# Kernel optimization log

Measured on AMD Instinct MI355X. Metric: run time of the kernel, lower is better.

Reference implementation:

```python
import jax, jax.numpy as jnp
import numpy as np

N_EDGES = 2_000_000
IN, HID, OUT = 10, 128, 4

# 4-bit narrow signed weight range: [-7, 7]; 4-bit unsigned act range: [0, 15]
W_QMAX = 7.0
A_QMAX = 15.0


def quant_weight(W):
    # NarrowIntQuant + MaxStatsScaling: per-tensor scale = max|W| / 7
    s = jnp.max(jnp.abs(W)) / W_QMAX
    return jnp.clip(jnp.round(W / s), -W_QMAX, W_QMAX) * s


def quant_act_relu(x, s):
    # QuantReLU with UintQuant: relu then uint4 fake-quant with per-tensor scale s
    x = jax.nn.relu(x)
    return jnp.clip(jnp.round(x / s), 0.0, A_QMAX) * s


def setup_inputs() -> dict:
    key = jax.random.key(0)
    ks = jax.random.split(key, 9)
    m = jax.random.normal(ks[0], (N_EDGES, IN), dtype=jnp.float32)
    W1 = jax.random.normal(ks[1], (HID, IN), dtype=jnp.float32) * (1.0 / np.sqrt(IN))
    b1 = jax.random.normal(ks[2], (HID,), dtype=jnp.float32) * 0.01
    W2 = jax.random.normal(ks[3], (HID, HID), dtype=jnp.float32) * (1.0 / np.sqrt(HID))
    b2 = jax.random.normal(ks[4], (HID,), dtype=jnp.float32) * 0.01
    W3 = jax.random.normal(ks[5], (OUT, HID), dtype=jnp.float32) * (1.0 / np.sqrt(HID))
    b3 = jax.random.normal(ks[6], (OUT,), dtype=jnp.float32) * 0.01
    # runtime-percentile act scales ~ typical pre-act magnitude / 15
    s_act1 = jax.random.uniform(ks[7], (1,), dtype=jnp.float32, minval=0.05, maxval=0.3)
    s_act2 = jax.random.uniform(ks[8], (1,), dtype=jnp.float32, minval=0.05, maxval=0.3)
    return {"m": m, "W1": W1, "b1": b1, "W2": W2, "b2": b2,
            "W3": W3, "b3": b3, "s_act1": s_act1, "s_act2": s_act2}


def reference(m, W1, b1, W2, b2, W3, b3, s_act1, s_act2):
    h = m @ quant_weight(W1).T + b1                 # [N, HID]
    h = quant_act_relu(h, s_act1[0])
    h = h @ quant_weight(W2).T + b2                 # [N, HID]
    h = quant_act_relu(h, s_act2[0])
    out = h @ quant_weight(W3).T + b3               # [N, OUT]
    return out
```

## Files before the change

### kernel.cpp

```cpp
#include <hip/hip_runtime.h>

#define IN 10
#define HID 128
#define OUT 4

__device__ float g_W1qf[HID * IN];
__device__ float g_W2qf[HID * HID];
__device__ float g_W3qf[OUT * HID];

__device__ __forceinline__ float f_fma(float a, float b, float c) {
    float d; asm("v_fma_f32 %0, %1, %2, %3" : "=v"(d) : "v"(a), "v"(b), "v"(c)); return d;
}
__device__ __forceinline__ float f_fma_s(float a, float w, float c) {
    float d; asm("v_fma_f32 %0, %1, %2, %3" : "=v"(d) : "v"(a), "s"(w), "v"(c)); return d;
}
__device__ __forceinline__ float f_mul(float a, float b) {
    float d; asm("v_mul_f32 %0, %1, %2" : "=v"(d) : "v"(a), "v"(b)); return d;
}
__device__ __forceinline__ float f_add(float a, float b) {
    float d; asm("v_add_f32 %0, %1, %2" : "=v"(d) : "v"(a), "v"(b)); return d;
}
__device__ __forceinline__ float f_sub(float a, float b) {
    float d; asm("v_sub_f32 %0, %1, %2" : "=v"(d) : "v"(a), "v"(b)); return d;
}
__device__ __forceinline__ float f_rndne(float a) {
    float d; asm("v_rndne_f32 %0, %1" : "=v"(d) : "v"(a)); return d;
}
__device__ __forceinline__ float f_rcp(float a) {
    float d; asm("v_rcp_f32 %0, %1" : "=v"(d) : "v"(a)); return d;
}
__device__ __forceinline__ float cvt_ub0(unsigned int u) {
    float d; asm("v_cvt_f32_ubyte0 %0, %1" : "=v"(d) : "v"(u)); return d;
}
__device__ __forceinline__ float cvt_ub1(unsigned int u) {
    float d; asm("v_cvt_f32_ubyte1 %0, %1" : "=v"(d) : "v"(u)); return d;
}
__device__ __forceinline__ float cvt_ub2(unsigned int u) {
    float d; asm("v_cvt_f32_ubyte2 %0, %1" : "=v"(d) : "v"(u)); return d;
}
__device__ __forceinline__ float cvt_ub3(unsigned int u) {
    float d; asm("v_cvt_f32_ubyte3 %0, %1" : "=v"(d) : "v"(u)); return d;
}

struct DivCR { float y, ns; };
__device__ __forceinline__ DivCR make_div(float s) {
    DivCR d;
    d.ns = f_sub(0.0f, s);
    float y0 = f_rcp(s);
    float e0 = f_fma(d.ns, y0, 1.0f);
    float y1 = f_fma(e0, y0, y0);
    float e1 = f_fma(d.ns, y1, 1.0f);
    d.y = f_fma(e1, y1, y1);
    return d;
}
__device__ __forceinline__ float div_cr(float h, DivCR d) {
    float q0 = f_mul(h, d.y);
    float r  = f_fma(d.ns, q0, h);
    return f_fma(r, d.y, q0);
}

__global__ void prep_kernel(const float* __restrict__ W1,
                            const float* __restrict__ W2,
                            const float* __restrict__ W3) {
    __shared__ float red[256];
    __shared__ float sS;
    const int t = threadIdx.x;
    const int which = blockIdx.x;

    const float* W; float* Wo; int n;
    if (which == 0)      { W = W1; Wo = g_W1qf; n = HID * IN; }
    else if (which == 1) { W = W2; Wo = g_W2qf; n = HID * HID; }
    else                 { W = W3; Wo = g_W3qf; n = OUT * HID; }

    float mx = 0.f;
    for (int i = t; i < n; i += 256) mx = fmaxf(mx, fabsf(W[i]));
    red[t] = mx;
    __syncthreads();
    for (int s = 128; s > 0; s >>= 1) {
        if (t < s) red[t] = fmaxf(red[t], red[t + s]);
        __syncthreads();
    }
    if (t == 0) {
        DivCR d7 = make_div(7.0f);
        sS = div_cr(red[0], d7);
    }
    __syncthreads();
    const float s = sS;
    const float rs = make_div(s).y;

    for (int i = t; i < n; i += 256) {
        float r = f_rndne(f_mul(W[i], rs));
        r = fminf(7.f, fmaxf(-7.f, r));
        Wo[i] = f_mul(r, s);
    }
}

__device__ __forceinline__ unsigned int quant_code(float acc, float bias, float recip) {
    float h = f_add(acc, bias);
    float r = f_rndne(f_mul(h, recip));
    r = fminf(15.f, fmaxf(0.f, r));
    return (unsigned int)r;
}

__global__ __launch_bounds__(512, 4) void mlp_kernel(
    const float* __restrict__ m,
    const float* __restrict__ b1,
    const float* __restrict__ b2,
    const float* __restrict__ b3,
    const float* __restrict__ s_act1,
    const float* __restrict__ s_act2,
    float* __restrict__ out, int nrows)
{
    __shared__ float sW2[HID * HID];

    const int t = threadIdx.x;

    {
        const float4* src = (const float4*)g_W2qf;
        float4* dst = (float4*)sW2;
        #pragma unroll
        for (int i = 0; i < 8; ++i) dst[t + 512 * i] = src[t + 512 * i];
    }
    __syncthreads();

    const int row = blockIdx.x * 512 + t;
    if (row >= nrows) return;

    const float s1 = s_act1[0];
    const float s2 = s_act2[0];
    const float r1 = make_div(s1).y;
    const float r2 = make_div(s2).y;

    float x[IN];
    const float2* mr = (const float2*)(m + (size_t)row * IN);
    #pragma unroll
    for (int i = 0; i < 5; ++i) {
        float2 v = mr[i];
        x[2 * i] = v.x; x[2 * i + 1] = v.y;
    }

    unsigned int actw[32];
    #pragma unroll
    for (int g = 0; g < 32; ++g) {
        const float* w0 = &g_W1qf[(4 * g + 0) * IN];
        const float* w1 = &g_W1qf[(4 * g + 1) * IN];
        const float* w2 = &g_W1qf[(4 * g + 2) * IN];
        const float* w3 = &g_W1qf[(4 * g + 3) * IN];
        float a0 = f_fma_s(x[0], w0[0], 0.0f);
        float a1c = f_fma_s(x[0], w1[0], 0.0f);
        float a2c = f_fma_s(x[0], w2[0], 0.0f);
        float a3c = f_fma_s(x[0], w3[0], 0.0f);
        #pragma unroll
        for (int k = 1; k < IN; ++k) {
            a0  = f_fma_s(x[k], w0[k], a0);
            a1c = f_fma_s(x[k], w1[k], a1c);
            a2c = f_fma_s(x[k], w2[k], a2c);
            a3c = f_fma_s(x[k], w3[k], a3c);
        }
        unsigned int c0 = quant_code(a0,  b1[4 * g + 0], r1);
        unsigned int c1 = quant_code(a1c, b1[4 * g + 1], r1);
        unsigned int c2 = quant_code(a2c, b1[4 * g + 2], r1);
        unsigned int c3 = quant_code(a3c, b1[4 * g + 3], r1);
        actw[g] = c0 | (c1 << 8) | (c2 << 16) | (c3 << 24);
        __builtin_amdgcn_sched_barrier(0);
    }

    float o0 = 0.0f, o1 = 0.0f, o2 = 0.0f, o3 = 0.0f;

    #pragma unroll 1
    for (int g = 0; g < 32; ++g) {
        const float4* w0 = (const float4*)&sW2[(4 * g + 0) * HID];
        const float4* w1 = (const float4*)&sW2[(4 * g + 1) * HID];
        const float4* w2 = (const float4*)&sW2[(4 * g + 2) * HID];
        const float4* w3 = (const float4*)&sW2[(4 * g + 3) * HID];
        float a0 = 0.0f, a1c = 0.0f, a2c = 0.0f, a3c = 0.0f;
        #pragma unroll
        for (int kp = 0; kp < 16; ++kp) {
            #pragma unroll
            for (int kh = 0; kh < 2; ++kh) {
                const int kk = 2 * kp + kh;
                float4 q0 = w0[kk];
                float4 q1 = w1[kk];
                float4 q2 = w2[kk];
                float4 q3 = w3[kk];
                const unsigned int u = actw[kk];
                float v0 = f_mul(cvt_ub0(u), s1);
                float v1 = f_mul(cvt_ub1(u), s1);
                float v2 = f_mul(cvt_ub2(u), s1);
                float v3 = f_mul(cvt_ub3(u), s1);
                a0  = f_fma(v0, q0.x, a0);
                a1c = f_fma(v0, q1.x, a1c);
                a2c = f_fma(v0, q2.x, a2c);
                a3c = f_fma(v0, q3.x, a3c);
                a0  = f_fma(v1, q0.y, a0);
                a1c = f_fma(v1, q1.y, a1c);
                a2c = f_fma(v1, q2.y, a2c);
                a3c = f_fma(v1, q3.y, a3c);
                a0  = f_fma(v2, q0.z, a0);
                a1c = f_fma(v2, q1.z, a1c);
                a2c = f_fma(v2, q2.z, a2c);
                a3c = f_fma(v2, q3.z, a3c);
                a0  = f_fma(v3, q0.w, a0);
                a1c = f_fma(v3, q1.w, a1c);
                a2c = f_fma(v3, q2.w, a2c);
                a3c = f_fma(v3, q3.w, a3c);
            }
            __builtin_amdgcn_sched_barrier(0);
        }
        unsigned int c0 = quant_code(a0,  b2[4 * g + 0], r2);
        unsigned int c1 = quant_code(a1c, b2[4 * g + 1], r2);
        unsigned int c2 = quant_code(a2c, b2[4 * g + 2], r2);
        unsigned int c3 = quant_code(a3c, b2[4 * g + 3], r2);
        float v0 = f_mul((float)c0, s2);
        float v1 = f_mul((float)c1, s2);
        float v2 = f_mul((float)c2, s2);
        float v3 = f_mul((float)c3, s2);
        o0 = f_fma_s(v0, g_W3qf[0 * HID + 4 * g + 0], o0);
        o1 = f_fma_s(v0, g_W3qf[1 * HID + 4 * g + 0], o1);
        o2 = f_fma_s(v0, g_W3qf[2 * HID + 4 * g + 0], o2);
        o3 = f_fma_s(v0, g_W3qf[3 * HID + 4 * g + 0], o3);
        o0 = f_fma_s(v1, g_W3qf[0 * HID + 4 * g + 1], o0);
        o1 = f_fma_s(v1, g_W3qf[1 * HID + 4 * g + 1], o1);
        o2 = f_fma_s(v1, g_W3qf[2 * HID + 4 * g + 1], o2);
        o3 = f_fma_s(v1, g_W3qf[3 * HID + 4 * g + 1], o3);
        o0 = f_fma_s(v2, g_W3qf[0 * HID + 4 * g + 2], o0);
        o1 = f_fma_s(v2, g_W3qf[1 * HID + 4 * g + 2], o1);
        o2 = f_fma_s(v2, g_W3qf[2 * HID + 4 * g + 2], o2);
        o3 = f_fma_s(v2, g_W3qf[3 * HID + 4 * g + 2], o3);
        o0 = f_fma_s(v3, g_W3qf[0 * HID + 4 * g + 3], o0);
        o1 = f_fma_s(v3, g_W3qf[1 * HID + 4 * g + 3], o1);
        o2 = f_fma_s(v3, g_W3qf[2 * HID + 4 * g + 3], o2);
        o3 = f_fma_s(v3, g_W3qf[3 * HID + 4 * g + 3], o3);
    }

    float4 o;
    o.x = f_add(o0, b3[0]);
    o.y = f_add(o1, b3[1]);
    o.z = f_add(o2, b3[2]);
    o.w = f_add(o3, b3[3]);
    *(float4*)(out + (size_t)row * OUT) = o;
}

extern "C" void kernel_launch(void* const* d_in, const int* in_sizes, int n_in,
                              void* d_out, int out_size, void* d_ws, size_t ws_size,
                              hipStream_t stream) {
    const float* m  = (const float*)d_in[0];
    const float* W1 = (const float*)d_in[1];
    const float* b1 = (const float*)d_in[2];
    const float* W2 = (const float*)d_in[3];
    const float* b2 = (const float*)d_in[4];
    const float* W3 = (const float*)d_in[5];
    const float* b3 = (const float*)d_in[6];
    const float* s1 = (const float*)d_in[7];
    const float* s2 = (const float*)d_in[8];
    const int nrows = in_sizes[0] / IN;

    prep_kernel<<<3, 256, 0, stream>>>(W1, W2, W3);
    const int nblk = (nrows + 511) / 512;
    mlp_kernel<<<nblk, 512, 0, stream>>>(m, b1, b2, b3, s1, s2, (float*)d_out, nrows);
}
```

Measured before the change: 1.172 ms.

## Process two rows per thread using packed FP32 FMA instructions

Each thread now handles two rows (A and B), packing their activations into float2 lanes and using v_pk_fma_f32/v_pk_mul_f32 with op_sel to broadcast weights. The intent is to double FMA throughput per instruction and halve the LDS weight reads per row, since each W2 load now serves two rows. The cost is twice the activation registers (two 32-word arrays), which may lower occupancy. The grid is halved and tail rows are clamped for loads and masked on store.

```diff
diff --git a/kernel.cpp b/kernel.cpp
--- a/kernel.cpp
+++ b/kernel.cpp
@@ -11,9 +11,6 @@
 __device__ __forceinline__ float f_fma(float a, float b, float c) {
     float d; asm("v_fma_f32 %0, %1, %2, %3" : "=v"(d) : "v"(a), "v"(b), "v"(c)); return d;
 }
-__device__ __forceinline__ float f_fma_s(float a, float w, float c) {
-    float d; asm("v_fma_f32 %0, %1, %2, %3" : "=v"(d) : "v"(a), "s"(w), "v"(c)); return d;
-}
 __device__ __forceinline__ float f_mul(float a, float b) {
     float d; asm("v_mul_f32 %0, %1, %2" : "=v"(d) : "v"(a), "v"(b)); return d;
 }
@@ -41,6 +38,19 @@
 __device__ __forceinline__ float cvt_ub3(unsigned int u) {
     float d; asm("v_cvt_f32_ubyte3 %0, %1" : "=v"(d) : "v"(u)); return d;
 }
+
+__device__ __forceinline__ void pk_fma_lo(float2& c, float2 a, float2 b) {
+    asm("v_pk_fma_f32 %0, %1, %2, %0 op_sel_hi:[1,0,1]" : "+v"(c) : "v"(a), "v"(b));
+}
+__device__ __forceinline__ void pk_fma_hi(float2& c, float2 a, float2 b) {
+    asm("v_pk_fma_f32 %0, %1, %2, %0 op_sel:[0,1,0] op_sel_hi:[1,1,1]" : "+v"(c) : "v"(a), "v"(b));
+}
+__device__ __forceinline__ float2 pk_mul_lo(float2 a, float2 b) {
+    float2 d; asm("v_pk_mul_f32 %0, %1, %2 op_sel_hi:[1,0]" : "=v"(d) : "v"(a), "v"(b));
+    return d;
+}
+__device__ __forceinline__ float2 lo2(float4 q) { return make_float2(q.x, q.y); }
+__device__ __forceinline__ float2 hi2(float4 q) { return make_float2(q.z, q.w); }
 
 struct DivCR { float y, ns; };
 __device__ __forceinline__ DivCR make_div(float s) {
@@ -123,49 +133,64 @@
     }
     __syncthreads();
 
-    const int row = blockIdx.x * 512 + t;
-    if (row >= nrows) return;
+    const int rowA = blockIdx.x * 1024 + t;
+    const int rowB = rowA + 512;
+    const int rA = rowA < nrows ? rowA : (nrows - 1);
+    const int rB = rowB < nrows ? rowB : (nrows - 1);
 
     const float s1 = s_act1[0];
     const float s2 = s_act2[0];
     const float r1 = make_div(s1).y;
     const float r2 = make_div(s2).y;
-
-    float x[IN];
-    const float2* mr = (const float2*)(m + (size_t)row * IN);
-    #pragma unroll
-    for (int i = 0; i < 5; ++i) {
-        float2 v = mr[i];
-        x[2 * i] = v.x; x[2 * i + 1] = v.y;
-    }
-
-    unsigned int actw[32];
+    float2 s1p; s1p.x = s1; s1p.y = s1;
+    float2 s2p; s2p.x = s2; s2p.y = s2;
+
+    float2 xp[IN];
+    {
+        const float2* ma = (const float2*)(m + (size_t)rA * IN);
+        const float2* mb = (const float2*)(m + (size_t)rB * IN);
+        #pragma unroll
+        for (int i = 0; i < 5; ++i) {
+            float2 va = ma[i], vb = mb[i];
+            xp[2 * i].x     = va.x; xp[2 * i].y     = vb.x;
+            xp[2 * i + 1].x = va.y; xp[2 * i + 1].y = vb.y;
+        }
+    }
+
+    unsigned int actwA[32], actwB[32];
     #pragma unroll
     for (int g = 0; g < 32; ++g) {
-        const float* w0 = &g_W1qf[(4 * g + 0) * IN];
-        const float* w1 = &g_W1qf[(4 * g + 1) * IN];
-        const float* w2 = &g_W1qf[(4 * g + 2) * IN];
-        const float* w3 = &g_W1qf[(4 * g + 3) * IN];
-        float a0 = f_fma_s(x[0], w0[0], 0.0f);
-        float a1c = f_fma_s(x[0], w1[0], 0.0f);
-        float a2c = f_fma_s(x[0], w2[0], 0.0f);
-        float a3c = f_fma_s(x[0], w3[0], 0.0f);
+        const float2* w0p = (const float2*)&g_W1qf[(4 * g + 0) * IN];
+        const float2* w1p = (const float2*)&g_W1qf[(4 * g + 1) * IN];
+        const float2* w2p = (const float2*)&g_W1qf[(4 * g + 2) * IN];
+        const float2* w3p = (const float2*)&g_W1qf[(4 * g + 3) * IN];
+        float2 a0 = make_float2(0.f, 0.f), a1c = a0, a2c = a0, a3c = a0;
         #pragma unroll
-        for (int k = 1; k < IN; ++k) {
-            a0  = f_fma_s(x[k], w0[k], a0);
-            a1c = f_fma_s(x[k], w1[k], a1c);
-            a2c = f_fma_s(x[k], w2[k], a2c);
-            a3c = f_fma_s(x[k], w3[k], a3c);
+        for (int kp = 0; kp < 5; ++kp) {
+            float2 wq0 = w0p[kp], wq1 = w1p[kp], wq2 = w2p[kp], wq3 = w3p[kp];
+            pk_fma_lo(a0,  xp[2 * kp],     wq0);
+            pk_fma_hi(a0,  xp[2 * kp + 1], wq0);
+            pk_fma_lo(a1c, xp[2 * kp],     wq1);
+            pk_fma_hi(a1c, xp[2 * kp + 1], wq1);
+            pk_fma_lo(a2c, xp[2 * kp],     wq2);
+            pk_fma_hi(a2c, xp[2 * kp + 1], wq2);
+            pk_fma_lo(a3c, xp[2 * kp],     wq3);
+            pk_fma_hi(a3c, xp[2 * kp + 1], wq3);
         }
-        unsigned int c0 = quant_code(a0,  b1[4 * g + 0], r1);
-        unsigned int c1 = quant_code(a1c, b1[4 * g + 1], r1);
-        unsigned int c2 = quant_code(a2c, b1[4 * g + 2], r1);
-        unsigned int c3 = quant_code(a3c, b1[4 * g + 3], r1);
-        actw[g] = c0 | (c1 << 8) | (c2 << 16) | (c3 << 24);
+        unsigned int cA0 = quant_code(a0.x,  b1[4 * g + 0], r1);
+        unsigned int cA1 = quant_code(a1c.x, b1[4 * g + 1], r1);
+        unsigned int cA2 = quant_code(a2c.x, b1[4 * g + 2], r1);
+        unsigned int cA3 = quant_code(a3c.x, b1[4 * g + 3], r1);
+        actwA[g] = cA0 | (cA1 << 8) | (cA2 << 16) | (cA3 << 24);
+        unsigned int cB0 = quant_code(a0.y,  b1[4 * g + 0], r1);
+        unsigned int cB1 = quant_code(a1c.y, b1[4 * g + 1], r1);
+        unsigned int cB2 = quant_code(a2c.y, b1[4 * g + 2], r1);
+        unsigned int cB3 = quant_code(a3c.y, b1[4 * g + 3], r1);
+        actwB[g] = cB0 | (cB1 << 8) | (cB2 << 16) | (cB3 << 24);
         __builtin_amdgcn_sched_barrier(0);
     }
 
-    float o0 = 0.0f, o1 = 0.0f, o2 = 0.0f, o3 = 0.0f;
+    float2 o0 = make_float2(0.f, 0.f), o1 = o0, o2 = o0, o3 = o0;
 
     #pragma unroll 1
     for (int g = 0; g < 32; ++g) {
@@ -173,72 +198,104 @@
         const float4* w1 = (const float4*)&sW2[(4 * g + 1) * HID];
         const float4* w2 = (const float4*)&sW2[(4 * g + 2) * HID];
         const float4* w3 = (const float4*)&sW2[(4 * g + 3) * HID];
-        float a0 = 0.0f, a1c = 0.0f, a2c = 0.0f, a3c = 0.0f;
+        float2 a0 = make_float2(0.f, 0.f), a1c = a0, a2c = a0, a3c = a0;
         #pragma unroll
-        for (int kp = 0; kp < 16; ++kp) {
-            #pragma unroll
-            for (int kh = 0; kh < 2; ++kh) {
-                const int kk = 2 * kp + kh;
-                float4 q0 = w0[kk];
-                float4 q1 = w1[kk];
-                float4 q2 = w2[kk];
-                float4 q3 = w3[kk];
-                const unsigned int u = actw[kk];
-                float v0 = f_mul(cvt_ub0(u), s1);
-                float v1 = f_mul(cvt_ub1(u), s1);
-                float v2 = f_mul(cvt_ub2(u), s1);
-                float v3 = f_mul(cvt_ub3(u), s1);
-                a0  = f_fma(v0, q0.x, a0);
-                a1c = f_fma(v0, q1.x, a1c);
-                a2c = f_fma(v0, q2.x, a2c);
-                a3c = f_fma(v0, q3.x, a3c);
-                a0  = f_fma(v1, q0.y, a0);
-                a1c = f_fma(v1, q1.y, a1c);
-                a2c = f_fma(v1, q2.y, a2c);
-                a3c = f_fma(v1, q3.y, a3c);
-                a0  = f_fma(v2, q0.z, a0);
-                a1c = f_fma(v2, q1.z, a1c);
-                a2c = f_fma(v2, q2.z, a2c);
-                a3c = f_fma(v2, q3.z, a3c);
-                a0  = f_fma(v3, q0.w, a0);
-                a1c = f_fma(v3, q1.w, a1c);
-                a2c = f_fma(v3, q2.w, a2c);
-                a3c = f_fma(v3, q3.w, a3c);
-            }
+        for (int kk = 0; kk < 32; ++kk) {
+            float4 q0 = w0[kk];
+            float4 q1 = w1[kk];
+            float4 q2 = w2[kk];
+            float4 q3 = w3[kk];
+            const unsigned int uA = actwA[kk];
+            const unsigned int uB = actwB[kk];
+            float2 cv0, cv1, cv2, cv3;
+            cv0.x = cvt_ub0(uA); cv0.y = cvt_ub0(uB);
+            cv1.x = cvt_ub1(uA); cv1.y = cvt_ub1(uB);
+            cv2.x = cvt_ub2(uA); cv2.y = cvt_ub2(uB);
+            cv3.x = cvt_ub3(uA); cv3.y = cvt_ub3(uB);
+            float2 av0 = pk_mul_lo(cv0, s1p);
+            float2 av1 = pk_mul_lo(cv1, s1p);
+            float2 av2 = pk_mul_lo(cv2, s1p);
+            float2 av3 = pk_mul_lo(cv3, s1p);
+            float2 q0l = lo2(q0), q0h = hi2(q0);
+            float2 q1l = lo2(q1), q1h = hi2(q1);
+            float2 q2l = lo2(q2), q2h = hi2(q2);
+            float2 q3l = lo2(q3), q3h = hi2(q3);
+            pk_fma_lo(a0,  av0, q0l);
+            pk_fma_hi(a0,  av1, q0l);
+            pk_fma_lo(a0,  av2, q0h);
+            pk_fma_hi(a0,  av3, q0h);
+            pk_fma_lo(a1c, av0, q1l);
+            pk_fma_hi(a1c, av1, q1l);
+            pk_fma_lo(a1c, av2, q1h);
+            pk_fma_hi(a1c, av3, q1h);
+            pk_fma_lo(a2c, av0, q2l);
+            pk_fma_hi(a2c, av1, q2l);
+            pk_fma_lo(a2c, av2, q2h);
+            pk_fma_hi(a2c, av3, q2h);
+            pk_fma_lo(a3c, av0, q3l);
+            pk_fma_hi(a3c, av1, q3l);
+            pk_fma_lo(a3c, av2, q3h);
+            pk_fma_hi(a3c, av3, q3h);
             __builtin_amdgcn_sched_barrier(0);
         }
-        unsigned int c0 = quant_code(a0,  b2[4 * g + 0], r2);
-        unsigned int c1 = quant_code(a1c, b2[4 * g + 1], r2);
-        unsigned int c2 = quant_code(a2c, b2[4 * g + 2], r2);
-        unsigned int c3 = quant_code(a3c, b2[4 * g + 3], r2);
-        float v0 = f_mul((float)c0, s2);
-        float v1 = f_mul((float)c1, s2);
-        float v2 = f_mul((float)c2, s2);
-        float v3 = f_mul((float)c3, s2);
-        o0 = f_fma_s(v0, g_W3qf[0 * HID + 4 * g + 0], o0);
-        o1 = f_fma_s(v0, g_W3qf[1 * HID + 4 * g + 0], o1);
-        o2 = f_fma_s(v0, g_W3qf[2 * HID + 4 * g + 0], o2);
-        o3 = f_fma_s(v0, g_W3qf[3 * HID + 4 * g + 0], o3);
-        o0 = f_fma_s(v1, g_W3qf[0 * HID + 4 * g + 1], o0);
-        o1 = f_fma_s(v1, g_W3qf[1 * HID + 4 * g + 1], o1);
-        o2 = f_fma_s(v1, g_W3qf[2 * HID + 4 * g + 1], o2);
-        o3 = f_fma_s(v1, g_W3qf[3 * HID + 4 * g + 1], o3);
-        o0 = f_fma_s(v2, g_W3qf[0 * HID + 4 * g + 2], o0);
-        o1 = f_fma_s(v2, g_W3qf[1 * HID + 4 * g + 2], o1);
-        o2 = f_fma_s(v2, g_W3qf[2 * HID + 4 * g + 2], o2);
-        o3 = f_fma_s(v2, g_W3qf[3 * HID + 4 * g + 2], o3);
-        o0 = f_fma_s(v3, g_W3qf[0 * HID + 4 * g + 3], o0);
-        o1 = f_fma_s(v3, g_W3qf[1 * HID + 4 * g + 3], o1);
-        o2 = f_fma_s(v3, g_W3qf[2 * HID + 4 * g + 3], o2);
-        o3 = f_fma_s(v3, g_W3qf[3 * HID + 4 * g + 3], o3);
-    }
-
-    float4 o;
-    o.x = f_add(o0, b3[0]);
-    o.y = f_add(o1, b3[1]);
-    o.z = f_add(o2, b3[2]);
-    o.w = f_add(o3, b3[3]);
-    *(float4*)(out + (size_t)row * OUT) = o;
+        unsigned int cA0 = quant_code(a0.x,  b2[4 * g + 0], r2);
+        unsigned int cA1 = quant_code(a1c.x, b2[4 * g + 1], r2);
+        unsigned int cA2 = quant_code(a2c.x, b2[4 * g + 2], r2);
+        unsigned int cA3 = quant_code(a3c.x, b2[4 * g + 3], r2);
+        unsigned int cB0 = quant_code(a0.y,  b2[4 * g + 0], r2);
+        unsigned int cB1 = quant_code(a1c.y, b2[4 * g + 1], r2);
+        unsigned int cB2 = quant_code(a2c.y, b2[4 * g + 2], r2);
+        unsigned int cB3 = quant_code(a3c.y, b2[4 * g + 3], r2);
+        float2 cp0; cp0.x = (float)cA0; cp0.y = (float)cB0;
+        float2 cp1; cp1.x = (float)cA1; cp1.y = (float)cB1;
+        float2 cp2; cp2.x = (float)cA2; cp2.y = (float)cB2;
+        float2 cp3; cp3.x = (float)cA3; cp3.y = (float)cB3;
+        float2 vp0 = pk_mul_lo(cp0, s2p);
+        float2 vp1 = pk_mul_lo(cp1, s2p);
+        float2 vp2 = pk_mul_lo(cp2, s2p);
+        float2 vp3 = pk_mul_lo(cp3, s2p);
+        const float2* u0p = (const float2*)&g_W3qf[0 * HID + 4 * g];
+        const float2* u1p = (const float2*)&g_W3qf[1 * HID + 4 * g];
+        const float2* u2p = (const float2*)&g_W3qf[2 * HID + 4 * g];
+        const float2* u3p = (const float2*)&g_W3qf[3 * HID + 4 * g];
+        float2 u0a = u0p[0], u0b = u0p[1];
+        float2 u1a = u1p[0], u1b = u1p[1];
+        float2 u2a = u2p[0], u2b = u2p[1];
+        float2 u3a = u3p[0], u3b = u3p[1];
+        pk_fma_lo(o0, vp0, u0a);
+        pk_fma_hi(o0, vp1, u0a);
+        pk_fma_lo(o0, vp2, u0b);
+        pk_fma_hi(o0, vp3, u0b);
+        pk_fma_lo(o1, vp0, u1a);
+        pk_fma_hi(o1, vp1, u1a);
+        pk_fma_lo(o1, vp2, u1b);
+        pk_fma_hi(o1, vp3, u1b);
+        pk_fma_lo(o2, vp0, u2a);
+        pk_fma_hi(o2, vp1, u2a);
+        pk_fma_lo(o2, vp2, u2b);
+        pk_fma_hi(o2, vp3, u2b);
+        pk_fma_lo(o3, vp0, u3a);
+        pk_fma_hi(o3, vp1, u3a);
+        pk_fma_lo(o3, vp2, u3b);
+        pk_fma_hi(o3, vp3, u3b);
+    }
+
+    if (rowA < nrows) {
+        float4 o;
+        o.x = f_add(o0.x, b3[0]);
+        o.y = f_add(o1.x, b3[1]);
+        o.z = f_add(o2.x, b3[2]);
+        o.w = f_add(o3.x, b3[3]);
+        *(float4*)(out + (size_t)rowA * OUT) = o;
+    }
+    if (rowB < nrows) {
+        float4 o;
+        o.x = f_add(o0.y, b3[0]);
+        o.y = f_add(o1.y, b3[1]);
+        o.z = f_add(o2.y, b3[2]);
+        o.w = f_add(o3.y, b3[3]);
+        *(float4*)(out + (size_t)rowB * OUT) = o;
+    }
 }
 
 extern "C" void kernel_launch(void* const* d_in, const int* in_sizes, int n_in,
@@ -256,6 +313,6 @@
     const int nrows = in_sizes[0] / IN;
 
     prep_kernel<<<3, 256, 0, stream>>>(W1, W2, W3);
-    const int nblk = (nrows + 511) / 512;
+    const int nblk = (nrows + 1023) / 1024;
     mlp_kernel<<<nblk, 512, 0, stream>>>(m, b1, b2, b3, s1, s2, (float*)d_out, nrows);
 }
```

Measured after the change: 1.236 ms. 5.5% more time.
